# Kernel tuning notes

Hardware: AMD Instinct MI355X
Metric: run time of the kernel (lower is better)

The kernel has to match this reference:

```python
import jax, jax.numpy as jnp
import numpy as np

N_HEADS = 8

def setup_inputs() -> dict:
    key = jax.random.key(0)
    qkv = jax.random.normal(key, (4, 1, 3 * N_HEADS * 64, 2048), dtype=jnp.float32)
    return {"qkv": qkv}

def reference(qkv):
    # qkv: [N, G, 3*H*C, T]
    bs, groups, width, length = qkv.shape
    ch = width // (3 * N_HEADS)
    q, k, v = jnp.split(qkv, 3, axis=2)
    scale = 1.0 / np.sqrt(ch)  # applied to BOTH q and k (as in original)
    qr = (q * scale).reshape(bs, groups, N_HEADS, ch, length)
    kr = (k * scale).reshape(bs, groups, N_HEADS, ch, length)
    vr = v.reshape(bs, groups, N_HEADS, ch, length)
    weight = jnp.einsum('bghct,bghcs->bghts', qr, kr)  # [N,G,H,T,T]
    weight = jax.nn.softmax(weight.astype(jnp.float32), axis=-1).astype(qkv.dtype)
    a = jnp.einsum('bghts,bghcs->bghct', weight, vr)  # [N,G,H,C,T]
    return a.reshape(bs, -1, length)  # [N, G*H*C, T]
```

## Files before the change

kernel.cpp:

```cpp
#include <hip/hip_runtime.h>
#include <hip/hip_bf16.h>

typedef __attribute__((ext_vector_type(4))) float f32x4;
typedef __attribute__((ext_vector_type(16))) float f32x16;
typedef __attribute__((ext_vector_type(4))) float f4;
typedef __attribute__((ext_vector_type(8))) short bf16x8;
typedef __attribute__((ext_vector_type(4))) short s16x4;
typedef __attribute__((ext_vector_type(8))) short s16x8;
typedef __attribute__((ext_vector_type(4))) unsigned u32x4;

#define T_LEN 2048
#define SPAD 72
#define QSCALE 0.022542110013890054f

#define SWZ(r) (((r) ^ ((r) >> 3)) & 7)

__device__ inline short f2bf(float f) {
  unsigned u = __builtin_bit_cast(unsigned, f);
  return (short)((u + 0x7fffu + ((u >> 16) & 1u)) >> 16);
}

__global__ __launch_bounds__(256) void prep(const float* __restrict__ qkv,
                                            short* __restrict__ kt,
                                            short* __restrict__ vb) {
  __shared__ float tile[64][65];
  const int bid = blockIdx.x;
  const int tid = threadIdx.x;

  if (bid < 1024) {
    const int tch = bid & 31;
    const int head = bid >> 5;
    const int b = head >> 3, h = head & 7;
    const float* src = qkv + ((size_t)b * 1536 + 512 + h * 64) * T_LEN + tch * 64;
    short* dst = kt + (size_t)head * 131072 + (size_t)tch * 4096;

    for (int e = tid; e < 4096; e += 256) {
      int c = e >> 6, t = e & 63;
      tile[c][t] = src[(size_t)c * T_LEN + t];
    }
    __syncthreads();
    for (int e = tid; e < 2048; e += 256) {
      int t = e >> 5, c2 = (e & 31) * 2;
      unsigned lo = (unsigned short)f2bf(tile[c2][t]);
      unsigned hi = (unsigned short)f2bf(tile[c2 + 1][t]);
      int cdst = c2 ^ (SWZ(t) << 3);
      *(unsigned*)&dst[t * 64 + cdst] = lo | (hi << 16);
    }
  } else {
    int id = (bid - 1024) * 256 + tid;
    int s8 = id & 7;
    int c = (id >> 3) & 63;
    int stile = (id >> 9) & 31;
    int head = id >> 14;
    int b = head >> 3, h = head & 7;
    const float* src =
        qkv + ((size_t)b * 1536 + 1024 + h * 64 + c) * T_LEN + stile * 64 + s8 * 8;
    f4 sA = *(const f4*)src;
    f4 sB = *(const f4*)(src + 4);
    s16x8 o;
#pragma unroll
    for (int j = 0; j < 4; ++j) { o[j] = f2bf(sA[j]); o[4 + j] = f2bf(sB[j]); }
    size_t dsts =
        (((size_t)head * 32 + stile) * 64 + c) * 64 + ((s8 * 8) ^ (SWZ(c) << 3));
    *(s16x8*)&vb[dsts] = o;
  }
}

__global__ __launch_bounds__(512, 4) void attn15(const float* __restrict__ qkv,
                                                 const short* __restrict__ Kt,
                                                 const short* __restrict__ Vb,
                                                 float* __restrict__ out) {
  __shared__ short KV[2][2][2][4096];

  const int bid = blockIdx.x;
  const int head = bid & 31;
  const int qblk = bid >> 5;

  const int tid = threadIdx.x;
  const int wave = tid >> 6;
  const int grp = wave >> 2;
  const int wv = wave & 3;
  const int lane = tid & 63;
  const int l31 = lane & 31;
  const int hi = lane >> 5;

  const int t0 = qblk * 128 + wv * 32;
  const int sbase = grp * 16;

  const int b = head >> 3, h = head & 7;
  const float* Qf = qkv + ((size_t)b * 1536 + h * 64) * T_LEN;
  const short* Kh = Kt + (size_t)head * 131072;
  const short* Vh = Vb + (size_t)head * 131072;
  float* O = out + (size_t)head * 131072;

  const int sw0 = SWZ(l31) << 3;
  const int sw1 = SWZ(l31 + 32) << 3;

  auto stage = [&](int buf, int it) {
#pragma unroll
    for (int j = 0; j < 4; ++j) {
      const int chunk = wv * 4 + j;
      const short* g =
          (chunk < 8 ? Kh : Vh) + (sbase + it) * 4096 + (chunk & 7) * 512 + lane * 8;
      short* l = &KV[grp][buf][chunk >> 3][(chunk & 7) * 512];
      __builtin_amdgcn_global_load_lds((const __attribute__((address_space(1))) void*)g,
                                       (__attribute__((address_space(3))) void*)l,
                                       16, 0, 0);
    }
  };

  stage(0, 0);

  bf16x8 aq[4];
#pragma unroll
  for (int ck = 0; ck < 4; ++ck) {
    float qv[8];
#pragma unroll
    for (int j = 0; j < 8; ++j)
      qv[j] = Qf[(size_t)(ck * 16 + hi * 8 + j) * T_LEN + t0 + l31];
#pragma unroll
    for (int j = 0; j < 8; ++j) aq[ck][j] = f2bf(qv[j] * QSCALE);
  }

  float l_lane = 0.f;
  f32x16 o_acc[2];
#pragma unroll
  for (int j = 0; j < 16; ++j) { o_acc[0][j] = 0.f; o_acc[1][j] = 0.f; }

  auto tile_body = [&](int buf) {
    f32x16 s0, s1;
#pragma unroll
    for (int j = 0; j < 16; ++j) { s0[j] = 0.f; s1[j] = 0.f; }
    __builtin_amdgcn_s_setprio(1);
#pragma unroll
    for (int ck = 0; ck < 4; ++ck) {
      const bf16x8 k0 = *(const bf16x8*)&KV[grp][buf][0][l31 * 64 + ((ck * 16 + hi * 8) ^ sw0)];
      s0 = __builtin_amdgcn_mfma_f32_32x32x16_bf16(k0, aq[ck], s0, 0, 0, 0);
      const bf16x8 k1 = *(const bf16x8*)&KV[grp][buf][0][(32 + l31) * 64 + ((ck * 16 + hi * 8) ^ sw1)];
      s1 = __builtin_amdgcn_mfma_f32_32x32x16_bf16(k1, aq[ck], s1, 0, 0, 0);
    }
    __builtin_amdgcn_s_setprio(0);

    float ps0 = 0.f, ps1 = 0.f, ps2 = 0.f, ps3 = 0.f;
    bf16x8 pf[4];
    const f32x16* sv[2] = {&s0, &s1};
#pragma unroll
    for (int sbk = 0; sbk < 2; ++sbk) {
      float p[16];
#pragma unroll
      for (int j = 0; j < 16; ++j) p[j] = __builtin_amdgcn_exp2f((*sv[sbk])[j]);
      ps0 += p[0] + p[4] + p[8] + p[12];
      ps1 += p[1] + p[5] + p[9] + p[13];
      ps2 += p[2] + p[6] + p[10] + p[14];
      ps3 += p[3] + p[7] + p[11] + p[15];
      unsigned w0, w1, w2, w3, w4, w5, w6, w7;
      asm("v_cvt_pk_bf16_f32 %0, %1, %2" : "=v"(w0) : "v"(p[0]), "v"(p[1]));
      asm("v_cvt_pk_bf16_f32 %0, %1, %2" : "=v"(w1) : "v"(p[2]), "v"(p[3]));
      asm("v_cvt_pk_bf16_f32 %0, %1, %2" : "=v"(w2) : "v"(p[4]), "v"(p[5]));
      asm("v_cvt_pk_bf16_f32 %0, %1, %2" : "=v"(w3) : "v"(p[6]), "v"(p[7]));
      asm("v_cvt_pk_bf16_f32 %0, %1, %2" : "=v"(w4) : "v"(p[8]), "v"(p[9]));
      asm("v_cvt_pk_bf16_f32 %0, %1, %2" : "=v"(w5) : "v"(p[10]), "v"(p[11]));
      asm("v_cvt_pk_bf16_f32 %0, %1, %2" : "=v"(w6) : "v"(p[12]), "v"(p[13]));
      asm("v_cvt_pk_bf16_f32 %0, %1, %2" : "=v"(w7) : "v"(p[14]), "v"(p[15]));
      asm("v_permlane32_swap_b32 %0, %1" : "+v"(w0), "+v"(w2));
      asm("v_permlane32_swap_b32 %0, %1" : "+v"(w1), "+v"(w3));
      asm("v_permlane32_swap_b32 %0, %1" : "+v"(w4), "+v"(w6));
      asm("v_permlane32_swap_b32 %0, %1" : "+v"(w5), "+v"(w7));
      u32x4 fe = {w0, w1, w2, w3};
      u32x4 fo = {w4, w5, w6, w7};
      pf[sbk * 2] = __builtin_bit_cast(bf16x8, fe);
      pf[sbk * 2 + 1] = __builtin_bit_cast(bf16x8, fo);
    }
    l_lane += (ps0 + ps1) + (ps2 + ps3);

    __builtin_amdgcn_s_setprio(1);
#pragma unroll
    for (int sc = 0; sc < 4; ++sc) {
      const bf16x8 v0 = *(const bf16x8*)&KV[grp][buf][1][l31 * 64 + ((sc * 16 + hi * 8) ^ sw0)];
      o_acc[0] = __builtin_amdgcn_mfma_f32_32x32x16_bf16(v0, pf[sc], o_acc[0], 0, 0, 0);
      const bf16x8 v1 = *(const bf16x8*)&KV[grp][buf][1][(32 + l31) * 64 + ((sc * 16 + hi * 8) ^ sw1)];
      o_acc[1] = __builtin_amdgcn_mfma_f32_32x32x16_bf16(v1, pf[sc], o_acc[1], 0, 0, 0);
    }
    __builtin_amdgcn_s_setprio(0);
  };

  __syncthreads();

  for (int itp = 0; itp < 8; ++itp) {
    const int it = itp * 2;
    stage(1, it + 1);
    tile_body(0);
    __syncthreads();
    if (itp < 7) stage(0, it + 2);
    tile_body(1);
    __syncthreads();
  }

  const float lg = l_lane + __shfl_xor(l_lane, 32, 64);
  float* xb = (float*)&KV[0][0][0][0];
  if (grp == 1) {
    float* dst = xb + (wv * 64 + lane) * 33;
#pragma unroll
    for (int j = 0; j < 16; ++j) { dst[j] = o_acc[0][j]; dst[16 + j] = o_acc[1][j]; }
    dst[32] = lg;
  }
  __syncthreads();
  if (grp == 0) {
    const float* src = xb + (wv * 64 + lane) * 33;
    const float rl = 1.0f / (lg + src[32]);
#pragma unroll
    for (int j = 0; j < 16; ++j) {
      const int c0 = (j & 3) + 8 * (j >> 2) + 4 * hi;
      O[(size_t)c0 * T_LEN + t0 + l31] = (o_acc[0][j] + src[j]) * rl;
      O[(size_t)(32 + c0) * T_LEN + t0 + l31] = (o_acc[1][j] + src[16 + j]) * rl;
    }
  }
}

__global__ __launch_bounds__(256) void attn_fwd(const float* __restrict__ qkv,
                                                float* __restrict__ out) {
  __shared__ short KtS[64][SPAD];
  __shared__ short VtS[64][SPAD];
  __shared__ short PbS[4][16][SPAD];

  const int bid = blockIdx.x;
  const int qt = bid & 31;
  const int head = bid >> 5;
  const int b = head >> 3, h = head & 7;

  const size_t base = ((size_t)b * 1536 + h * 64) * T_LEN;
  const float* Q = qkv + base;
  const float* K = qkv + base + (size_t)512 * T_LEN;
  const float* V = qkv + base + (size_t)1024 * T_LEN;
  float* O = out + ((size_t)b * 512 + h * 64) * T_LEN;

  const int tid = threadIdx.x;
  const int wave = tid >> 6;
  const int lane = tid & 63;
  const int l15 = lane & 15;
  const int l4 = lane >> 4;
  const int t0 = qt * 64 + wave * 16;

  bf16x8 aq[2];
#pragma unroll
  for (int kk = 0; kk < 2; ++kk)
#pragma unroll
    for (int j = 0; j < 8; ++j) {
      int c = kk * 32 + l4 * 8 + j;
      aq[kk][j] = f2bf(Q[(size_t)c * T_LEN + t0 + l15]);
    }

  float m_run[4], l_run[4];
  f32x4 o_acc[4];
#pragma unroll
  for (int r = 0; r < 4; ++r) { m_run[r] = -1e30f; l_run[r] = 0.f; }
#pragma unroll
  for (int n = 0; n < 4; ++n) o_acc[n] = (f32x4){0.f, 0.f, 0.f, 0.f};

  const float inv64 = 0.015625f;

  for (int s0 = 0; s0 < T_LEN; s0 += 64) {
    __syncthreads();
    for (int e = tid; e < 4096; e += 256) {
      int c = e >> 6, s = e & 63;
      KtS[s][c] = f2bf(K[(size_t)c * T_LEN + s0 + s]);
      VtS[c][s] = f2bf(V[(size_t)c * T_LEN + s0 + s]);
    }
    __syncthreads();

    f32x4 sacc[4];
#pragma unroll
    for (int n = 0; n < 4; ++n) {
      const bf16x8 bk0 = *(const bf16x8*)&KtS[16 * n + l15][l4 * 8];
      const bf16x8 bk1 = *(const bf16x8*)&KtS[16 * n + l15][32 + l4 * 8];
      f32x4 z = (f32x4){0.f, 0.f, 0.f, 0.f};
      z = __builtin_amdgcn_mfma_f32_16x16x32_bf16(aq[0], bk0, z, 0, 0, 0);
      z = __builtin_amdgcn_mfma_f32_16x16x32_bf16(aq[1], bk1, z, 0, 0, 0);
      sacc[n] = z;
    }

#pragma unroll
    for (int r = 0; r < 4; ++r) {
      float mx = fmaxf(fmaxf(sacc[0][r], sacc[1][r]),
                       fmaxf(sacc[2][r], sacc[3][r])) * inv64;
#pragma unroll
      for (int off = 8; off >= 1; off >>= 1)
        mx = fmaxf(mx, __shfl_xor(mx, off, 64));
      const float m_new = fmaxf(m_run[r], mx);
      const float alpha = __expf(m_run[r] - m_new);
      float psum = 0.f;
#pragma unroll
      for (int n = 0; n < 4; ++n) {
        float p = __expf(sacc[n][r] * inv64 - m_new);
        psum += p;
        PbS[wave][l4 * 4 + r][16 * n + l15] = f2bf(p);
      }
#pragma unroll
      for (int off = 8; off >= 1; off >>= 1)
        psum += __shfl_xor(psum, off, 64);
      l_run[r] = l_run[r] * alpha + psum;
      m_run[r] = m_new;
#pragma unroll
      for (int n = 0; n < 4; ++n) o_acc[n][r] *= alpha;
    }

    const bf16x8 ap0 = *(const bf16x8*)&PbS[wave][l15][l4 * 8];
    const bf16x8 ap1 = *(const bf16x8*)&PbS[wave][l15][32 + l4 * 8];
#pragma unroll
    for (int n = 0; n < 4; ++n) {
      const bf16x8 bv0 = *(const bf16x8*)&VtS[16 * n + l15][l4 * 8];
      const bf16x8 bv1 = *(const bf16x8*)&VtS[16 * n + l15][32 + l4 * 8];
      o_acc[n] = __builtin_amdgcn_mfma_f32_16x16x32_bf16(ap0, bv0, o_acc[n], 0, 0, 0);
      o_acc[n] = __builtin_amdgcn_mfma_f32_16x16x32_bf16(ap1, bv1, o_acc[n], 0, 0, 0);
    }
  }

#pragma unroll
  for (int n = 0; n < 4; ++n)
#pragma unroll
    for (int r = 0; r < 4; ++r) {
      const int c = 16 * n + l15;
      const int t = t0 + l4 * 4 + r;
      O[(size_t)c * T_LEN + t] = o_acc[n][r] / l_run[r];
    }
}

extern "C" void kernel_launch(void* const* d_in, const int* in_sizes, int n_in,
                              void* d_out, int out_size, void* d_ws, size_t ws_size,
                              hipStream_t stream) {
  const float* qkv = (const float*)d_in[0];
  float* out = (float*)d_out;
  const size_t per_buf = (size_t)32 * T_LEN * 64;
  const size_t need_kv = per_buf * 2 * sizeof(short);
  if (ws_size >= need_kv) {
    short* kt = (short*)d_ws;
    short* vb = kt + per_buf;
    hipLaunchKernelGGL(prep, dim3(3072), dim3(256), 0, stream, qkv, kt, vb);
    hipLaunchKernelGGL(attn15, dim3(512), dim3(512), 0, stream, qkv, kt, vb, out);
  } else {
    hipLaunchKernelGGL(attn_fwd, dim3(1024), dim3(256), 0, stream, qkv, out);
  }
}
```

Baseline: 53.69 us.

## Quantize Q and K to FP8 E4M3 and use FP8 MFMA for scores

Q and K are converted to FP8 E4M3 in software, with Q pre-scaled by a larger factor. The QK^T product now uses fp8 MFMA instructions, and the lost scale is restored before exp2. The K workspace and its LDS staging halve in size with a new swizzled byte layout, while V stays in bf16. The aim is less K bandwidth and LDS traffic and cheaper score MFMAs, at the cost of lower precision in the attention logits and a more expensive per-element software conversion in prep and on the Q load.

```diff
diff --git a/kernel.cpp b/kernel.cpp
--- a/kernel.cpp
+++ b/kernel.cpp
@@ -5,12 +5,13 @@
 typedef __attribute__((ext_vector_type(16))) float f32x16;
 typedef __attribute__((ext_vector_type(4))) float f4;
 typedef __attribute__((ext_vector_type(8))) short bf16x8;
-typedef __attribute__((ext_vector_type(4))) short s16x4;
 typedef __attribute__((ext_vector_type(8))) short s16x8;
+typedef __attribute__((ext_vector_type(2))) unsigned u32x2;
 typedef __attribute__((ext_vector_type(4))) unsigned u32x4;
 
 #define T_LEN 2048
 #define SPAD 72
+#define QS8 0.7213475204444817f
 #define QSCALE 0.022542110013890054f
 
 #define SWZ(r) (((r) ^ ((r) >> 3)) & 7)
@@ -20,8 +21,29 @@
   return (short)((u + 0x7fffu + ((u >> 16) & 1u)) >> 16);
 }
 
+__device__ inline unsigned f2e4m3(float f) {
+  unsigned u = __builtin_bit_cast(unsigned, f);
+  unsigned s = (u >> 24) & 0x80u;
+  int e = (int)((u >> 23) & 0xff) - 127;
+  if (e >= -6) {
+    unsigned m = u & 0x7fffffu;
+    unsigned mant = m >> 20;
+    unsigned rest = m & 0xfffffu;
+    mant += (rest > 0x80000u || (rest == 0x80000u && (mant & 1u))) ? 1u : 0u;
+    return s | (((unsigned)(e + 7) << 3) + mant);
+  }
+  if (e < -10) return s;
+  unsigned full = 0x800000u | (u & 0x7fffffu);
+  int rs = 14 - e;
+  unsigned mant = full >> rs;
+  unsigned rest = full & ((1u << rs) - 1u);
+  unsigned half = 1u << (rs - 1);
+  mant += (rest > half || (rest == half && (mant & 1u))) ? 1u : 0u;
+  return s | mant;
+}
+
 __global__ __launch_bounds__(256) void prep(const float* __restrict__ qkv,
-                                            short* __restrict__ kt,
+                                            unsigned char* __restrict__ kt,
                                             short* __restrict__ vb) {
   __shared__ float tile[64][65];
   const int bid = blockIdx.x;
@@ -32,19 +54,26 @@
     const int head = bid >> 5;
     const int b = head >> 3, h = head & 7;
     const float* src = qkv + ((size_t)b * 1536 + 512 + h * 64) * T_LEN + tch * 64;
-    short* dst = kt + (size_t)head * 131072 + (size_t)tch * 4096;
+    unsigned char* dst = kt + (size_t)head * 131072 + (size_t)tch * 4096;
 
     for (int e = tid; e < 4096; e += 256) {
       int c = e >> 6, t = e & 63;
       tile[c][t] = src[(size_t)c * T_LEN + t];
     }
     __syncthreads();
-    for (int e = tid; e < 2048; e += 256) {
-      int t = e >> 5, c2 = (e & 31) * 2;
-      unsigned lo = (unsigned short)f2bf(tile[c2][t]);
-      unsigned hi = (unsigned short)f2bf(tile[c2 + 1][t]);
-      int cdst = c2 ^ (SWZ(t) << 3);
-      *(unsigned*)&dst[t * 64 + cdst] = lo | (hi << 16);
+    for (int e = tid; e < 512; e += 256) {
+      int row = e >> 3, grp = e & 7;
+      int hi = grp >> 2, ck = grp & 3;
+      int cbase = ck * 16 + hi * 8;
+      unsigned b0 = 0, b1 = 0;
+#pragma unroll
+      for (int j = 0; j < 4; ++j) b0 |= f2e4m3(tile[cbase + j][row]) << (8 * j);
+#pragma unroll
+      for (int j = 0; j < 4; ++j) b1 |= f2e4m3(tile[cbase + 4 + j][row]) << (8 * j);
+      int off = row * 64 + (((hi << 5) + ((ck & 2) << 3)) ^ (((row >> 1) & 3) << 4)) +
+                ((ck & 1) << 3);
+      u32x2 w = {b0, b1};
+      *(u32x2*)&dst[off] = w;
     }
   } else {
     int id = (bid - 1024) * 256 + tid;
@@ -66,11 +95,11 @@
   }
 }
 
-__global__ __launch_bounds__(512, 4) void attn15(const float* __restrict__ qkv,
-                                                 const short* __restrict__ Kt,
+__global__ __launch_bounds__(512, 4) void attn18(const float* __restrict__ qkv,
+                                                 const unsigned char* __restrict__ Kt,
                                                  const short* __restrict__ Vb,
                                                  float* __restrict__ out) {
-  __shared__ short KV[2][2][2][4096];
+  __shared__ __align__(16) unsigned char SM[2][2][12288];
 
   const int bid = blockIdx.x;
   const int head = bid & 31;
@@ -89,37 +118,53 @@
 
   const int b = head >> 3, h = head & 7;
   const float* Qf = qkv + ((size_t)b * 1536 + h * 64) * T_LEN;
-  const short* Kh = Kt + (size_t)head * 131072;
+  const unsigned char* Kh = Kt + (size_t)head * 131072;
   const short* Vh = Vb + (size_t)head * 131072;
   float* O = out + (size_t)head * 131072;
 
   const int sw0 = SWZ(l31) << 3;
   const int sw1 = SWZ(l31 + 32) << 3;
+  const int kswz = ((l31 >> 1) & 3) << 4;
+  const int koffA = (hi << 5) ^ kswz;
+  const int koffB = ((hi << 5) + 16) ^ kswz;
 
   auto stage = [&](int buf, int it) {
 #pragma unroll
-    for (int j = 0; j < 4; ++j) {
-      const int chunk = wv * 4 + j;
-      const short* g =
-          (chunk < 8 ? Kh : Vh) + (sbase + it) * 4096 + (chunk & 7) * 512 + lane * 8;
-      short* l = &KV[grp][buf][chunk >> 3][(chunk & 7) * 512];
-      __builtin_amdgcn_global_load_lds((const __attribute__((address_space(1))) void*)g,
-                                       (__attribute__((address_space(3))) void*)l,
-                                       16, 0, 0);
+    for (int j = 0; j < 3; ++j) {
+      const int chunk = wv * 3 + j;
+      if (chunk < 4) {
+        const unsigned char* g =
+            Kh + (size_t)(sbase + it) * 4096 + chunk * 1024 + lane * 16;
+        unsigned char* l = &SM[grp][buf][chunk * 1024];
+        __builtin_amdgcn_global_load_lds((const __attribute__((address_space(1))) void*)g,
+                                         (__attribute__((address_space(3))) void*)l,
+                                         16, 0, 0);
+      } else {
+        const short* g =
+            Vh + (size_t)(sbase + it) * 4096 + (chunk - 4) * 512 + lane * 8;
+        unsigned char* l = &SM[grp][buf][4096 + (chunk - 4) * 1024];
+        __builtin_amdgcn_global_load_lds((const __attribute__((address_space(1))) void*)g,
+                                         (__attribute__((address_space(3))) void*)l,
+                                         16, 0, 0);
+      }
     }
   };
 
   stage(0, 0);
 
-  bf16x8 aq[4];
+  long bq[4];
 #pragma unroll
   for (int ck = 0; ck < 4; ++ck) {
     float qv[8];
 #pragma unroll
     for (int j = 0; j < 8; ++j)
       qv[j] = Qf[(size_t)(ck * 16 + hi * 8 + j) * T_LEN + t0 + l31];
-#pragma unroll
-    for (int j = 0; j < 8; ++j) aq[ck][j] = f2bf(qv[j] * QSCALE);
+    unsigned b0 = 0, b1 = 0;
+#pragma unroll
+    for (int j = 0; j < 4; ++j) b0 |= f2e4m3(qv[j] * QS8) << (8 * j);
+#pragma unroll
+    for (int j = 0; j < 4; ++j) b1 |= f2e4m3(qv[4 + j] * QS8) << (8 * j);
+    bq[ck] = (long)(((unsigned long)b1 << 32) | b0);
   }
 
   float l_lane = 0.f;
@@ -128,16 +173,34 @@
   for (int j = 0; j < 16; ++j) { o_acc[0][j] = 0.f; o_acc[1][j] = 0.f; }
 
   auto tile_body = [&](int buf) {
+    const unsigned char* Kp = &SM[grp][buf][0];
+    const short* Vp = (const short*)&SM[grp][buf][4096];
+
     f32x16 s0, s1;
 #pragma unroll
     for (int j = 0; j < 16; ++j) { s0[j] = 0.f; s1[j] = 0.f; }
     __builtin_amdgcn_s_setprio(1);
-#pragma unroll
-    for (int ck = 0; ck < 4; ++ck) {
-      const bf16x8 k0 = *(const bf16x8*)&KV[grp][buf][0][l31 * 64 + ((ck * 16 + hi * 8) ^ sw0)];
-      s0 = __builtin_amdgcn_mfma_f32_32x32x16_bf16(k0, aq[ck], s0, 0, 0, 0);
-      const bf16x8 k1 = *(const bf16x8*)&KV[grp][buf][0][(32 + l31) * 64 + ((ck * 16 + hi * 8) ^ sw1)];
-      s1 = __builtin_amdgcn_mfma_f32_32x32x16_bf16(k1, aq[ck], s1, 0, 0, 0);
+    {
+      const u32x4 a0 = *(const u32x4*)&Kp[l31 * 64 + koffA];
+      const u32x4 b0v = *(const u32x4*)&Kp[l31 * 64 + koffB];
+      const u32x4 a1 = *(const u32x4*)&Kp[(32 + l31) * 64 + koffA];
+      const u32x4 b1v = *(const u32x4*)&Kp[(32 + l31) * 64 + koffB];
+      s0 = __builtin_amdgcn_mfma_f32_32x32x16_fp8_fp8(
+          (long)(((unsigned long)a0[1] << 32) | a0[0]), bq[0], s0, 0, 0, 0);
+      s0 = __builtin_amdgcn_mfma_f32_32x32x16_fp8_fp8(
+          (long)(((unsigned long)a0[3] << 32) | a0[2]), bq[1], s0, 0, 0, 0);
+      s0 = __builtin_amdgcn_mfma_f32_32x32x16_fp8_fp8(
+          (long)(((unsigned long)b0v[1] << 32) | b0v[0]), bq[2], s0, 0, 0, 0);
+      s0 = __builtin_amdgcn_mfma_f32_32x32x16_fp8_fp8(
+          (long)(((unsigned long)b0v[3] << 32) | b0v[2]), bq[3], s0, 0, 0, 0);
+      s1 = __builtin_amdgcn_mfma_f32_32x32x16_fp8_fp8(
+          (long)(((unsigned long)a1[1] << 32) | a1[0]), bq[0], s1, 0, 0, 0);
+      s1 = __builtin_amdgcn_mfma_f32_32x32x16_fp8_fp8(
+          (long)(((unsigned long)a1[3] << 32) | a1[2]), bq[1], s1, 0, 0, 0);
+      s1 = __builtin_amdgcn_mfma_f32_32x32x16_fp8_fp8(
+          (long)(((unsigned long)b1v[1] << 32) | b1v[0]), bq[2], s1, 0, 0, 0);
+      s1 = __builtin_amdgcn_mfma_f32_32x32x16_fp8_fp8(
+          (long)(((unsigned long)b1v[3] << 32) | b1v[2]), bq[3], s1, 0, 0, 0);
     }
     __builtin_amdgcn_s_setprio(0);
 
@@ -148,7 +211,8 @@
     for (int sbk = 0; sbk < 2; ++sbk) {
       float p[16];
 #pragma unroll
-      for (int j = 0; j < 16; ++j) p[j] = __builtin_amdgcn_exp2f((*sv[sbk])[j]);
+      for (int j = 0; j < 16; ++j)
+        p[j] = __builtin_amdgcn_exp2f((*sv[sbk])[j] * 0.03125f);
       ps0 += p[0] + p[4] + p[8] + p[12];
       ps1 += p[1] + p[5] + p[9] + p[13];
       ps2 += p[2] + p[6] + p[10] + p[14];
@@ -176,9 +240,9 @@
     __builtin_amdgcn_s_setprio(1);
 #pragma unroll
     for (int sc = 0; sc < 4; ++sc) {
-      const bf16x8 v0 = *(const bf16x8*)&KV[grp][buf][1][l31 * 64 + ((sc * 16 + hi * 8) ^ sw0)];
+      const bf16x8 v0 = *(const bf16x8*)&Vp[l31 * 64 + ((sc * 16 + hi * 8) ^ sw0)];
       o_acc[0] = __builtin_amdgcn_mfma_f32_32x32x16_bf16(v0, pf[sc], o_acc[0], 0, 0, 0);
-      const bf16x8 v1 = *(const bf16x8*)&KV[grp][buf][1][(32 + l31) * 64 + ((sc * 16 + hi * 8) ^ sw1)];
+      const bf16x8 v1 = *(const bf16x8*)&Vp[(32 + l31) * 64 + ((sc * 16 + hi * 8) ^ sw1)];
       o_acc[1] = __builtin_amdgcn_mfma_f32_32x32x16_bf16(v1, pf[sc], o_acc[1], 0, 0, 0);
     }
     __builtin_amdgcn_s_setprio(0);
@@ -197,7 +261,7 @@
   }
 
   const float lg = l_lane + __shfl_xor(l_lane, 32, 64);
-  float* xb = (float*)&KV[0][0][0][0];
+  float* xb = (float*)&SM[0][0][0];
   if (grp == 1) {
     float* dst = xb + (wv * 64 + lane) * 33;
 #pragma unroll
@@ -330,13 +394,14 @@
                               hipStream_t stream) {
   const float* qkv = (const float*)d_in[0];
   float* out = (float*)d_out;
-  const size_t per_buf = (size_t)32 * T_LEN * 64;
-  const size_t need_kv = per_buf * 2 * sizeof(short);
-  if (ws_size >= need_kv) {
-    short* kt = (short*)d_ws;
-    short* vb = kt + per_buf;
+  const size_t kbytes = (size_t)32 * T_LEN * 64;
+  const size_t vshorts = (size_t)32 * T_LEN * 64;
+  const size_t need = kbytes + vshorts * sizeof(short);
+  if (ws_size >= need) {
+    unsigned char* kt = (unsigned char*)d_ws;
+    short* vb = (short*)(kt + kbytes);
     hipLaunchKernelGGL(prep, dim3(3072), dim3(256), 0, stream, qkv, kt, vb);
-    hipLaunchKernelGGL(attn15, dim3(512), dim3(512), 0, stream, qkv, kt, vb, out);
+    hipLaunchKernelGGL(attn18, dim3(512), dim3(512), 0, stream, qkv, kt, vb, out);
   } else {
     hipLaunchKernelGGL(attn_fwd, dim3(1024), dim3(256), 0, stream, qkv, out);
   }
```

Result: slower. 64.32 us (+19.8%).
